# Performance work log

Hardware: AMD Instinct MI355X
Metric: run time of the kernel (lower is better)

## Reference

```python
import jax, jax.numpy as jnp
import numpy as np

N_NODES = 100000
N_EDGES = 1600000
F_IN = 128
HEADS1, CH1 = 8, 16
N_CLASSES = 64
NEG_SLOPE = 0.2  # PyG GATConv default leaky-relu slope


def setup_inputs() -> dict:
    key = jax.random.key(0)
    ks = jax.random.split(key, 10)
    x = jax.random.normal(ks[0], (N_NODES, F_IN), dtype=jnp.float32)
    edge_index = jax.random.randint(ks[1], (2, N_EDGES), 0, N_NODES, dtype=jnp.int32)
    s1 = 1.0 / np.sqrt(F_IN)
    s2 = 1.0 / np.sqrt(HEADS1 * CH1)
    W1 = jax.random.normal(ks[2], (F_IN, HEADS1 * CH1), dtype=jnp.float32) * s1
    a_src1 = jax.random.normal(ks[3], (HEADS1, CH1), dtype=jnp.float32) * s2
    a_dst1 = jax.random.normal(ks[4], (HEADS1, CH1), dtype=jnp.float32) * s2
    b1 = jnp.zeros((HEADS1 * CH1,), dtype=jnp.float32)
    W2 = jax.random.normal(ks[5], (HEADS1 * CH1, N_CLASSES), dtype=jnp.float32) * s2
    a_src2 = jax.random.normal(ks[6], (1, N_CLASSES), dtype=jnp.float32) * 0.1
    a_dst2 = jax.random.normal(ks[7], (1, N_CLASSES), dtype=jnp.float32) * 0.1
    b2 = jnp.zeros((N_CLASSES,), dtype=jnp.float32)
    return {"x": x, "edge_index": edge_index, "W1": W1, "a_src1": a_src1,
            "a_dst1": a_dst1, "b1": b1, "W2": W2, "a_src2": a_src2,
            "a_dst2": a_dst2, "b2": b2}


def gat_layer(x, src, dst, W, a_src, a_dst, b, heads, ch, concat):
    # PyG GATConv (eval mode, self-loops already appended to src/dst).
    N = x.shape[0]
    h = (x @ W).reshape(N, heads, ch)                      # [N,H,C]
    asn = jnp.einsum('nhc,hc->nh', h, a_src)               # src attention term
    adn = jnp.einsum('nhc,hc->nh', h, a_dst)               # dst attention term
    e = jax.nn.leaky_relu(asn[src] + adn[dst], NEG_SLOPE)  # [E,H]
    emax = jax.ops.segment_max(e, dst, num_segments=N)     # per-dst max (self-loops guarantee nonempty)
    ee = jnp.exp(e - emax[dst])
    denom = jax.ops.segment_sum(ee, dst, num_segments=N)
    alpha = ee / denom[dst]                                # segment softmax over incoming edges
    msg = h[src] * alpha[:, :, None]                       # [E,H,C]
    out = jax.ops.segment_sum(msg, dst, num_segments=N)    # [N,H,C]
    out = out.reshape(N, heads * ch) if concat else out.mean(axis=1)
    return out + b


def reference(x, edge_index, W1, a_src1, a_dst1, b1, W2, a_src2, a_dst2, b2):
    N = x.shape[0]
    loop = jnp.arange(N, dtype=edge_index.dtype)
    src = jnp.concatenate([edge_index[0], loop])  # add self-loops (PyG default)
    dst = jnp.concatenate([edge_index[1], loop])
    h = gat_layer(x, src, dst, W1, a_src1, a_dst1, b1, HEADS1, CH1, True)
    h = jax.nn.elu(h)
    # F.dropout with training=False is identity (eval mode)
    out = gat_layer(h, src, dst, W2, a_src2, a_dst2, b2, 1, N_CLASSES, False)
    return jax.nn.log_softmax(out, axis=1)
```

## Files before the change

### kernel.cpp

```cpp
#include <hip/hip_runtime.h>

#define NN 100000
#define NE 1600000
#define EN (NE + NN)
#define FIN 128
#define H1 8
#define C1 16
#define F1 128
#define NC 64
#define NEG 0.2f

#define BSH 7
#define BKN 128
#define NBUK ((NN + BKN - 1) / BKN)
#define NBLK 256
#define CHUNK ((EN + NBLK - 1) / NBLK)
__device__ __forceinline__ int chunk_of_block(int b) {
  return (b & 7) * (NBLK / 8) + (b >> 3);
}

typedef unsigned short ushort_t;
typedef unsigned int uint_t;
typedef __attribute__((ext_vector_type(8))) short short8v;
typedef __attribute__((ext_vector_type(4))) float f32x4;
typedef __attribute__((ext_vector_type(2))) float f32x2;

union U8 { ushort_t u[8]; short8v v; uint4 q; };

__device__ __forceinline__ ushort_t f2bf(float f) {
  uint_t u = __builtin_bit_cast(uint_t, f);
  u += 0x7FFF + ((u >> 16) & 1);
  return (ushort_t)(u >> 16);
}
__device__ __forceinline__ float bflo(uint_t u) {
  return __builtin_bit_cast(float, u << 16);
}
__device__ __forceinline__ float bfhi(uint_t u) {
  return __builtin_bit_cast(float, u & 0xFFFF0000u);
}

#if __has_builtin(__builtin_amdgcn_cvt_pk_fp8_f32) && \
    __has_builtin(__builtin_amdgcn_cvt_pk_f32_fp8)
__device__ __forceinline__ uint_t fp8_pack4(float f0, float f1, float f2,
                                            float f3) {
  int p = 0;
  p = __builtin_amdgcn_cvt_pk_fp8_f32(f0, f1, p, false);
  p = __builtin_amdgcn_cvt_pk_fp8_f32(f2, f3, p, true);
  return (uint_t)p;
}
__device__ __forceinline__ void fp8_unpack4(uint_t w, float* o) {
  f32x2 d0 = __builtin_amdgcn_cvt_pk_f32_fp8((int)w, false);
  f32x2 d1 = __builtin_amdgcn_cvt_pk_f32_fp8((int)w, true);
  o[0] = d0.x; o[1] = d0.y; o[2] = d1.x; o[3] = d1.y;
}
#else
__device__ __forceinline__ uint_t fp8_enc1(float f) {
  uint_t u = __builtin_bit_cast(uint_t, f);
  uint_t s = (u >> 24) & 0x80u;
  int e = (int)((u >> 23) & 0xFF) - 127;
  if (e < -9) return s;
  if (e < -6) {
    float af = __builtin_bit_cast(float, u & 0x7FFFFFFFu);
    uint_t m = (uint_t)(af * 512.f + 0.5f);
    return s | m;
  }
  uint_t mant = u & 0x7FFFFF;
  uint_t keep = mant >> 20;
  uint_t rest = mant & 0xFFFFF;
  keep += (rest > 0x80000u) || (rest == 0x80000u && (keep & 1));
  uint_t ee = (uint_t)(e + 7);
  if (keep == 8) { keep = 0; ee += 1; }
  if (ee > 15 || (ee == 15 && keep > 6)) return s | 0x7E;
  return s | (ee << 3) | keep;
}
__device__ __forceinline__ float fp8_dec1(uint_t b) {
  uint_t s = (b & 0x80u) << 24;
  uint_t e = (b >> 3) & 15u, m = b & 7u;
  if (e == 0) {
    float v = (float)m * (1.0f / 512.0f);
    return __builtin_bit_cast(float, s | __builtin_bit_cast(uint_t, v));
  }
  return __builtin_bit_cast(float, s | ((e + 120u) << 23) | (m << 20));
}
__device__ __forceinline__ uint_t fp8_pack4(float f0, float f1, float f2,
                                            float f3) {
  return fp8_enc1(f0) | (fp8_enc1(f1) << 8) | (fp8_enc1(f2) << 16) |
         (fp8_enc1(f3) << 24);
}
__device__ __forceinline__ void fp8_unpack4(uint_t w, float* o) {
  o[0] = fp8_dec1(w & 0xFF); o[1] = fp8_dec1((w >> 8) & 0xFF);
  o[2] = fp8_dec1((w >> 16) & 0xFF); o[3] = fp8_dec1(w >> 24);
}
#endif

__global__ __launch_bounds__(512) void bucket_count_kernel(
    const int* __restrict__ dstA, int* __restrict__ cnt,
    const float* __restrict__ W1, const float* __restrict__ W2,
    ushort_t* __restrict__ WT1, ushort_t* __restrict__ WT2) {
  __shared__ int histL[NBUK];
  int b = blockIdx.x, t = threadIdx.x;
  int gid = b * 512 + t;
  if (gid < 128 * 128) {
    int n = gid >> 7, k = gid & 127;
    int c = (n & 15) * 8 + (n >> 4);
    WT1[gid] = f2bf(W1[k * 128 + c]);
  } else if (gid < 128 * 128 + 64 * 128) {
    int j = gid - 128 * 128;
    int n = j >> 7, k = j & 127;
    int c = (n & 15) * 4 + (n >> 4);
    WT2[j] = f2bf(W2[k * 64 + c]);
  }
  for (int i = t; i < NBUK; i += 512) histL[i] = 0;
  __syncthreads();
  int ch = chunk_of_block(b);
  int e0 = ch * CHUNK, e1 = min(e0 + CHUNK, EN);
  for (int e = e0 + t; e < e1; e += 512) {
    int d = (e < NE) ? dstA[e] : (e - NE);
    atomicAdd(&histL[d >> BSH], 1);
  }
  __syncthreads();
  for (int i = t; i < NBUK; i += 512) cnt[i * NBLK + ch] = histL[i];
}

__global__ __launch_bounds__(256) void scan_chunks_kernel(
    int* __restrict__ cnt, int* __restrict__ colsum) {
  __shared__ int sd[2][256];
  int j = blockIdx.x, t = threadIdx.x;
  int v = cnt[j * NBLK + t];
  sd[0][t] = v;
  __syncthreads();
  int sp = 0;
  for (int off = 1; off < 256; off <<= 1) {
    int val = sd[sp][t];
    if (t >= off) val += sd[sp][t - off];
    sd[sp ^ 1][t] = val;
    __syncthreads();
    sp ^= 1;
  }
  cnt[j * NBLK + t] = sd[sp][t] - v;
  if (t == 255) colsum[j] = sd[sp][255];
}

__global__ __launch_bounds__(1024) void scan_buckets_kernel(
    const int* __restrict__ colsum, int* __restrict__ bucket_base) {
  __shared__ int sd[2][1024];
  int t = threadIdx.x;
  int v = (t < NBUK) ? colsum[t] : 0;
  sd[0][t] = v;
  __syncthreads();
  int sp = 0;
  for (int off = 1; off < 1024; off <<= 1) {
    int val = sd[sp][t];
    if (t >= off) val += sd[sp][t - off];
    sd[sp ^ 1][t] = val;
    __syncthreads();
    sp ^= 1;
  }
  if (t < NBUK) bucket_base[t] = sd[sp][t] - v;
  if (t == 0) bucket_base[NBUK] = EN;
}

__global__ __launch_bounds__(512) void scatter_gemm1_kernel(
    const int* __restrict__ srcA, const int* __restrict__ dstA,
    const int* __restrict__ cnt, const int* __restrict__ bucket_base,
    int* __restrict__ staging,
    const float* __restrict__ X, const ushort_t* __restrict__ WT1,
    const float* __restrict__ a_src, const float* __restrict__ a_dst,
    uint2* __restrict__ h8, float* __restrict__ asn, float* __restrict__ adn,
    int nrows) {
  __shared__ int cur[NBUK];
  if (blockIdx.x < NBLK) {
    int b = blockIdx.x, t = threadIdx.x;
    int ch = chunk_of_block(b);
    for (int i = t; i < NBUK; i += 512)
      cur[i] = cnt[i * NBLK + ch] + bucket_base[i];
    __syncthreads();
    int e0 = ch * CHUNK, e1 = min(e0 + CHUNK, EN);
    for (int e = e0 + t; e < e1; e += 512) {
      int s, d;
      if (e < NE) { s = srcA[e]; d = dstA[e]; } else { s = e - NE; d = s; }
      int pos = atomicAdd(&cur[d >> BSH], 1);
      staging[pos] = s | ((d & (BKN - 1)) << 17);
    }
    return;
  }
  const int tid = threadIdx.x;
  const int wave = tid >> 6, lane = tid & 63;
  const int row0 = (blockIdx.x - NBLK) * 128 + wave * 16;
  const int rlo = lane & 15, khi = lane >> 4;

  f32x4 acc[8];
#pragma unroll
  for (int n = 0; n < 8; ++n) acc[n] = (f32x4){0.f, 0.f, 0.f, 0.f};

#pragma unroll
  for (int ks = 0; ks < 4; ++ks) {
    const int kk = ks * 32 + khi * 8;
    int row = row0 + rlo;
    if (row >= nrows) row = nrows - 1;
    const float4* xp = (const float4*)(X + (size_t)row * 128 + kk);
    float4 u = xp[0], v = xp[1];
    U8 t;
    t.u[0] = f2bf(u.x); t.u[1] = f2bf(u.y); t.u[2] = f2bf(u.z); t.u[3] = f2bf(u.w);
    t.u[4] = f2bf(v.x); t.u[5] = f2bf(v.y); t.u[6] = f2bf(v.z); t.u[7] = f2bf(v.w);
    short8v a = t.v;
#pragma unroll
    for (int nf = 0; nf < 8; ++nf) {
      short8v b = *(const short8v*)(WT1 + (nf * 16 + rlo) * 128 + kk);
      acc[nf] = __builtin_amdgcn_mfma_f32_16x16x32_bf16(a, b, acc[nf], 0, 0, 0);
    }
  }
  const float4* as4 = (const float4*)a_src;
  const float4* ad4 = (const float4*)a_dst;
  float4 as0 = as4[rlo * 2], as1 = as4[rlo * 2 + 1];
  float4 ad0 = ad4[rlo * 2], ad1 = ad4[rlo * 2 + 1];
  int rbase = row0 + khi * 4;
#pragma unroll
  for (int r = 0; r < 4; ++r) {
    int row = rbase + r;
    bool ok = (row < nrows);
    uint2 pk;
    pk.x = fp8_pack4(acc[0][r], acc[1][r], acc[2][r], acc[3][r]);
    pk.y = fp8_pack4(acc[4][r], acc[5][r], acc[6][r], acc[7][r]);
    if (ok) h8[(size_t)row * 16 + rlo] = pk;
    float s = acc[0][r] * as0.x + acc[1][r] * as0.y +
              acc[2][r] * as0.z + acc[3][r] * as0.w +
              acc[4][r] * as1.x + acc[5][r] * as1.y +
              acc[6][r] * as1.z + acc[7][r] * as1.w;
    float d = acc[0][r] * ad0.x + acc[1][r] * ad0.y +
              acc[2][r] * ad0.z + acc[3][r] * ad0.w +
              acc[4][r] * ad1.x + acc[5][r] * ad1.y +
              acc[6][r] * ad1.z + acc[7][r] * ad1.w;
    s += __shfl_xor(s, 1);
    d += __shfl_xor(d, 1);
    if (ok && (rlo & 1) == 0) {
      asn[row * 8 + (rlo >> 1)] = s;
      adn[row * 8 + (rlo >> 1)] = d;
    }
  }
}

__global__ __launch_bounds__(1024) void csr_gather1_kernel(
    const int* __restrict__ staging, const int* __restrict__ bucket_base,
    int* __restrict__ rp, int* __restrict__ col,
    const float* __restrict__ asn, const float* __restrict__ adn,
    const uint4* __restrict__ h8, const float* __restrict__ b1,
    ushort_t* __restrict__ x2) {
  __shared__ int degL[BKN];
  __shared__ int curL[BKN];
  __shared__ int startL[BKN + 1];
  __shared__ int sdata[2][BKN];
  int bk = blockIdx.x, t = threadIdx.x;
  int ebase = bucket_base[bk], eend = bucket_base[bk + 1];
  int ecnt = eend - ebase;
  if (t < BKN) degL[t] = 0;
  __syncthreads();
  for (int e = t; e < ecnt; e += 1024)
    atomicAdd(&degL[staging[ebase + e] >> 17], 1);
  __syncthreads();
  if (t < BKN) sdata[0][t] = degL[t];
  __syncthreads();
  int sp = 0;
  for (int off = 1; off < BKN; off <<= 1) {
    if (t < BKN) {
      int val = sdata[sp][t];
      if (t >= off) val += sdata[sp][t - off];
      sdata[sp ^ 1][t] = val;
    }
    __syncthreads();
    sp ^= 1;
  }
  if (t < BKN) {
    int ex = sdata[sp][t] - degL[t];
    curL[t] = ex;
    startL[t] = ebase + ex;
    int node = bk * BKN + t;
    if (node < NN) rp[node] = ebase + ex;
  }
  if (t == 0) startL[BKN] = eend;
  if (bk == 0 && t == 0) rp[NN] = EN;
  __syncthreads();
  for (int e = t; e < ecnt; e += 1024) {
    int pk = staging[ebase + e];
    int pos = atomicAdd(&curL[pk >> 17], 1);
    col[ebase + pos] = pk & 0x1FFFF;
  }
  __syncthreads();
  int i = t >> 3, lane = t & 7;
  int node = bk * BKN + i;
  if (node >= NN) return;
  float aD = adn[node * 8 + lane];
  int p = startL[i], p1 = startL[i + 1];
  float a[16];
#pragma unroll
  for (int j = 0; j < 16; ++j) a[j] = 0.f;
  float den = 0.f;
  for (; p + 1 < p1; p += 2) {
    int s0 = col[p], s1 = col[p + 1];
    float e0 = asn[s0 * 8 + lane] + aD;
    float e1 = asn[s1 * 8 + lane] + aD;
    uint4 q0 = h8[(size_t)s0 * 8 + lane];
    uint4 q1 = h8[(size_t)s1 * 8 + lane];
    e0 = e0 > 0.f ? e0 : NEG * e0;
    e1 = e1 > 0.f ? e1 : NEG * e1;
    float ee0 = __expf(e0), ee1 = __expf(e1);
    float d0[4], d1[4], d2[4], d3[4];
    fp8_unpack4(q0.x, d0); fp8_unpack4(q0.y, d1);
    fp8_unpack4(q0.z, d2); fp8_unpack4(q0.w, d3);
    float g0[4], g1[4], g2[4], g3[4];
    fp8_unpack4(q1.x, g0); fp8_unpack4(q1.y, g1);
    fp8_unpack4(q1.z, g2); fp8_unpack4(q1.w, g3);
#pragma unroll
    for (int j = 0; j < 4; ++j) {
      a[j]      += ee0 * d0[j] + ee1 * g0[j];
      a[4 + j]  += ee0 * d1[j] + ee1 * g1[j];
      a[8 + j]  += ee0 * d2[j] + ee1 * g2[j];
      a[12 + j] += ee0 * d3[j] + ee1 * g3[j];
    }
    den += ee0 + ee1;
  }
  if (p < p1) {
    int s0 = col[p];
    float e0 = asn[s0 * 8 + lane] + aD;
    uint4 q0 = h8[(size_t)s0 * 8 + lane];
    e0 = e0 > 0.f ? e0 : NEG * e0;
    float ee0 = __expf(e0);
    float d0[4], d1[4], d2[4], d3[4];
    fp8_unpack4(q0.x, d0); fp8_unpack4(q0.y, d1);
    fp8_unpack4(q0.z, d2); fp8_unpack4(q0.w, d3);
#pragma unroll
    for (int j = 0; j < 4; ++j) {
      a[j] += ee0 * d0[j];
      a[4 + j] += ee0 * d1[j];
      a[8 + j] += ee0 * d2[j];
      a[12 + j] += ee0 * d3[j];
    }
    den += ee0;
  }
  float inv = 1.f / den;
  const float4* b4 = (const float4*)b1;
  U8 t0, t1;
#pragma unroll
  for (int h = 0; h < 4; ++h) {
    float4 bv = b4[lane * 4 + h];
    float o0 = fmaf(a[h * 4 + 0], inv, bv.x);
    float o1 = fmaf(a[h * 4 + 1], inv, bv.y);
    float o2 = fmaf(a[h * 4 + 2], inv, bv.z);
    float o3 = fmaf(a[h * 4 + 3], inv, bv.w);
    o0 = o0 > 0.f ? o0 : __expf(o0) - 1.f;
    o1 = o1 > 0.f ? o1 : __expf(o1) - 1.f;
    o2 = o2 > 0.f ? o2 : __expf(o2) - 1.f;
    o3 = o3 > 0.f ? o3 : __expf(o3) - 1.f;
    U8& tt = (h < 2) ? t0 : t1;
    int base = (h & 1) * 4;
    tt.u[base + 0] = f2bf(o0); tt.u[base + 1] = f2bf(o1);
    tt.u[base + 2] = f2bf(o2); tt.u[base + 3] = f2bf(o3);
  }
  uint4* xr = (uint4*)(x2 + (size_t)node * F1);
  xr[lane * 2 + 0] = t0.q;
  xr[lane * 2 + 1] = t1.q;
}

__global__ __launch_bounds__(256) void mfma_gemm2_kernel(
    const ushort_t* __restrict__ X2, const ushort_t* __restrict__ WT2,
    const float* __restrict__ a_src, const float* __restrict__ a_dst,
    uint_t* __restrict__ h28, float* __restrict__ asn, float* __restrict__ adn,
    int nrows) {
  const int tid = threadIdx.x;
  const int wave = tid >> 6, lane = tid & 63;
  const int row0 = blockIdx.x * 64 + wave * 16;
  const int rlo = lane & 15, khi = lane >> 4;

  f32x4 acc[4];
#pragma unroll
  for (int n = 0; n < 4; ++n) acc[n] = (f32x4){0.f, 0.f, 0.f, 0.f};

#pragma unroll
  for (int ks = 0; ks < 4; ++ks) {
    const int kk = ks * 32 + khi * 8;
    int row = row0 + rlo;
    if (row >= nrows) row = nrows - 1;
    U8 t;
    t.q = *(const uint4*)(X2 + (size_t)row * 128 + kk);
    short8v a = t.v;
#pragma unroll
    for (int nf = 0; nf < 4; ++nf) {
      short8v b = *(const short8v*)(WT2 + (nf * 16 + rlo) * 128 + kk);
      acc[nf] = __builtin_amdgcn_mfma_f32_16x16x32_bf16(a, b, acc[nf], 0, 0, 0);
    }
  }
  float4 as = ((const float4*)a_src)[rlo];
  float4 ad = ((const float4*)a_dst)[rlo];
  int rbase = row0 + khi * 4;
#pragma unroll
  for (int r = 0; r < 4; ++r) {
    int row = rbase + r;
    bool ok = (row < nrows);
    uint_t pk = fp8_pack4(acc[0][r], acc[1][r], acc[2][r], acc[3][r]);
    if (ok) h28[(size_t)row * 16 + rlo] = pk;
    float s = acc[0][r] * as.x + acc[1][r] * as.y +
              acc[2][r] * as.z + acc[3][r] * as.w;
    float d = acc[0][r] * ad.x + acc[1][r] * ad.y +
              acc[2][r] * ad.z + acc[3][r] * ad.w;
    s += __shfl_xor(s, 1); s += __shfl_xor(s, 2);
    s += __shfl_xor(s, 4); s += __shfl_xor(s, 8);
    d += __shfl_xor(d, 1); d += __shfl_xor(d, 2);
    d += __shfl_xor(d, 4); d += __shfl_xor(d, 8);
    if (ok && rlo == 0) { asn[row] = s; adn[row] = d; }
  }
}

__global__ __launch_bounds__(256) void gather2_kernel(
    const int* __restrict__ rp, const int* __restrict__ col,
    const float* __restrict__ asn, const float* __restrict__ adn,
    const uint2* __restrict__ h28, const float* __restrict__ b2,
    float* __restrict__ out) {
  int node = (blockIdx.x << 5) + (threadIdx.x >> 3);
  if (node >= NN) return;
  int lane = threadIdx.x & 7;
  float aD = adn[node];
  int p = rp[node], p1 = rp[node + 1];
  float a[8];
#pragma unroll
  for (int j = 0; j < 8; ++j) a[j] = 0.f;
  float den = 0.f;

  for (; p + 1 < p1; p += 2) {
    int s0 = col[p], s1 = col[p + 1];
    float e0 = asn[s0] + aD;
    float e1 = asn[s1] + aD;
    uint2 q0 = h28[(size_t)s0 * 8 + lane];
    uint2 q1 = h28[(size_t)s1 * 8 + lane];
    e0 = e0 > 0.f ? e0 : NEG * e0;
    e1 = e1 > 0.f ? e1 : NEG * e1;
    float ee0 = __expf(e0), ee1 = __expf(e1);
    float d0[4], d1[4], g0[4], g1[4];
    fp8_unpack4(q0.x, d0); fp8_unpack4(q0.y, d1);
    fp8_unpack4(q1.x, g0); fp8_unpack4(q1.y, g1);
#pragma unroll
    for (int j = 0; j < 4; ++j) {
      a[j] += ee0 * d0[j] + ee1 * g0[j];
      a[4 + j] += ee0 * d1[j] + ee1 * g1[j];
    }
    den += ee0 + ee1;
  }
  if (p < p1) {
    int s0 = col[p];
    float e0 = asn[s0] + aD;
    uint2 q0 = h28[(size_t)s0 * 8 + lane];
    e0 = e0 > 0.f ? e0 : NEG * e0;
    float ee0 = __expf(e0);
    float d0[4], d1[4];
    fp8_unpack4(q0.x, d0); fp8_unpack4(q0.y, d1);
#pragma unroll
    for (int j = 0; j < 4; ++j) {
      a[j] += ee0 * d0[j];
      a[4 + j] += ee0 * d1[j];
    }
    den += ee0;
  }
  float inv = 1.f / den;
  float4 bv0 = ((const float4*)b2)[lane * 2 + 0];
  float4 bv1 = ((const float4*)b2)[lane * 2 + 1];
  float v[8];
  v[0] = fmaf(a[0], inv, bv0.x); v[1] = fmaf(a[1], inv, bv0.y);
  v[2] = fmaf(a[2], inv, bv0.z); v[3] = fmaf(a[3], inv, bv0.w);
  v[4] = fmaf(a[4], inv, bv1.x); v[5] = fmaf(a[5], inv, bv1.y);
  v[6] = fmaf(a[6], inv, bv1.z); v[7] = fmaf(a[7], inv, bv1.w);
  float m = v[0];
#pragma unroll
  for (int j = 1; j < 8; ++j) m = fmaxf(m, v[j]);
#pragma unroll
  for (int k = 1; k < 8; k <<= 1) m = fmaxf(m, __shfl_xor(m, k));
  float ex = 0.f;
#pragma unroll
  for (int j = 0; j < 8; ++j) ex += __expf(v[j] - m);
#pragma unroll
  for (int k = 1; k < 8; k <<= 1) ex += __shfl_xor(ex, k);
  float lse = m + __logf(ex);
  float4 r0 = {v[0] - lse, v[1] - lse, v[2] - lse, v[3] - lse};
  float4 r1 = {v[4] - lse, v[5] - lse, v[6] - lse, v[7] - lse};
  float4* orow = (float4*)(out + (size_t)node * NC);
  orow[lane * 2 + 0] = r0;
  orow[lane * 2 + 1] = r1;
}

extern "C" void kernel_launch(void* const* d_in, const int* in_sizes, int n_in,
                              void* d_out, int out_size, void* d_ws,
                              size_t ws_size, hipStream_t stream) {
  const float* x = (const float*)d_in[0];
  const int* edge_index = (const int*)d_in[1];
  const float* W1 = (const float*)d_in[2];
  const float* a_src1 = (const float*)d_in[3];
  const float* a_dst1 = (const float*)d_in[4];
  const float* b1 = (const float*)d_in[5];
  const float* W2 = (const float*)d_in[6];
  const float* a_src2 = (const float*)d_in[7];
  const float* a_dst2 = (const float*)d_in[8];
  const float* b2 = (const float*)d_in[9];
  float* out = (float*)d_out;
  float* ws = (float*)d_ws;

  ushort_t* x2b = (ushort_t*)ws;
  uint4* h8 = (uint4*)(ws + 6400000);
  uint2* h28 = (uint2*)(ws + 9600000);
  float* asn1 = ws + 11200000;
  float* adn1 = ws + 12000000;
  float* asn2 = ws + 12800000;
  float* adn2 = ws + 12900000;
  ushort_t* WT1 = (ushort_t*)(ws + 13000000);
  ushort_t* WT2 = (ushort_t*)(ws + 13010000);
  int* rp = (int*)(ws + 13020000);
  int* col = rp + NN + 1;
  int* staging = col + EN;
  int* cnt = staging + EN;
  int* bucket_base = cnt + NBUK * NBLK;
  int* colsum = bucket_base + NBUK + 1;

  const int* srcA = edge_index;
  const int* dstA = edge_index + NE;

  bucket_count_kernel<<<NBLK, 512, 0, stream>>>(dstA, cnt, W1, W2, WT1, WT2);
  scan_chunks_kernel<<<NBUK, 256, 0, stream>>>(cnt, colsum);
  scan_buckets_kernel<<<1, 1024, 0, stream>>>(colsum, bucket_base);
  scatter_gemm1_kernel<<<NBLK + (NN + 127) / 128, 512, 0, stream>>>(
      srcA, dstA, cnt, bucket_base, staging, x, WT1, a_src1, a_dst1,
      (uint2*)h8, asn1, adn1, NN);
  csr_gather1_kernel<<<NBUK, 1024, 0, stream>>>(staging, bucket_base, rp, col,
                                                asn1, adn1, h8, b1, x2b);
  mfma_gemm2_kernel<<<(NN + 63) / 64, 256, 0, stream>>>(
      x2b, WT2, a_src2, a_dst2, (uint_t*)h28, asn2, adn2, NN);
  gather2_kernel<<<(NN + 31) / 32, 256, 0, stream>>>(rp, col, asn2, adn2, h28,
                                                     b2, out);
}
```

Before: 189.0 us.

## Split scatter from GEMM1 and stage bucket CSR columns in LDS

Splits the fused scatter+GEMM1 kernel into two separate launches: a scatter kernel and a 256-thread GEMM1 kernel over 64-row tiles. In the CSR/gather kernel, each bucket's column list is built in shared memory when it fits (CAPB entries). The gather loop then reads source indices from LDS rather than re-reading global col. This is meant to remove the global round-trip of col and the scattered writes. In exchange it adds an extra kernel launch, loses the overlap between scatter and GEMM, and larger LDS use may lower occupancy of the 1024-thread blocks.

```diff
diff --git a/kernel.cpp b/kernel.cpp
--- a/kernel.cpp
+++ b/kernel.cpp
@@ -15,6 +15,7 @@
 #define NBUK ((NN + BKN - 1) / BKN)
 #define NBLK 256
 #define CHUNK ((EN + NBLK - 1) / NBLK)
+#define CAPB 2688
 __device__ __forceinline__ int chunk_of_block(int b) {
   return (b & 7) * (NBLK / 8) + (b >> 3);
 }
@@ -160,33 +161,33 @@
   if (t == 0) bucket_base[NBUK] = EN;
 }
 
-__global__ __launch_bounds__(512) void scatter_gemm1_kernel(
+__global__ __launch_bounds__(512) void bucket_scatter_kernel(
     const int* __restrict__ srcA, const int* __restrict__ dstA,
     const int* __restrict__ cnt, const int* __restrict__ bucket_base,
-    int* __restrict__ staging,
+    int* __restrict__ staging) {
+  __shared__ int cur[NBUK];
+  int b = blockIdx.x, t = threadIdx.x;
+  int ch = chunk_of_block(b);
+  for (int i = t; i < NBUK; i += 512)
+    cur[i] = cnt[i * NBLK + ch] + bucket_base[i];
+  __syncthreads();
+  int e0 = ch * CHUNK, e1 = min(e0 + CHUNK, EN);
+  for (int e = e0 + t; e < e1; e += 512) {
+    int s, d;
+    if (e < NE) { s = srcA[e]; d = dstA[e]; } else { s = e - NE; d = s; }
+    int pos = atomicAdd(&cur[d >> BSH], 1);
+    staging[pos] = s | ((d & (BKN - 1)) << 17);
+  }
+}
+
+__global__ __launch_bounds__(256) void mfma_gemm1_kernel(
     const float* __restrict__ X, const ushort_t* __restrict__ WT1,
     const float* __restrict__ a_src, const float* __restrict__ a_dst,
     uint2* __restrict__ h8, float* __restrict__ asn, float* __restrict__ adn,
     int nrows) {
-  __shared__ int cur[NBUK];
-  if (blockIdx.x < NBLK) {
-    int b = blockIdx.x, t = threadIdx.x;
-    int ch = chunk_of_block(b);
-    for (int i = t; i < NBUK; i += 512)
-      cur[i] = cnt[i * NBLK + ch] + bucket_base[i];
-    __syncthreads();
-    int e0 = ch * CHUNK, e1 = min(e0 + CHUNK, EN);
-    for (int e = e0 + t; e < e1; e += 512) {
-      int s, d;
-      if (e < NE) { s = srcA[e]; d = dstA[e]; } else { s = e - NE; d = s; }
-      int pos = atomicAdd(&cur[d >> BSH], 1);
-      staging[pos] = s | ((d & (BKN - 1)) << 17);
-    }
-    return;
-  }
   const int tid = threadIdx.x;
   const int wave = tid >> 6, lane = tid & 63;
-  const int row0 = (blockIdx.x - NBLK) * 128 + wave * 16;
+  const int row0 = blockIdx.x * 64 + wave * 16;
   const int rlo = lane & 15, khi = lane >> 4;
 
   f32x4 acc[8];
@@ -250,9 +251,11 @@
   __shared__ int curL[BKN];
   __shared__ int startL[BKN + 1];
   __shared__ int sdata[2][BKN];
+  __shared__ int colL[CAPB];
   int bk = blockIdx.x, t = threadIdx.x;
   int ebase = bucket_base[bk], eend = bucket_base[bk + 1];
   int ecnt = eend - ebase;
+  bool fits = (ecnt <= CAPB);
   if (t < BKN) degL[t] = 0;
   __syncthreads();
   for (int e = t; e < ecnt; e += 1024)
@@ -273,17 +276,28 @@
   if (t < BKN) {
     int ex = sdata[sp][t] - degL[t];
     curL[t] = ex;
-    startL[t] = ebase + ex;
+    startL[t] = ex;
     int node = bk * BKN + t;
     if (node < NN) rp[node] = ebase + ex;
   }
-  if (t == 0) startL[BKN] = eend;
+  if (t == 0) startL[BKN] = ecnt;
   if (bk == 0 && t == 0) rp[NN] = EN;
   __syncthreads();
-  for (int e = t; e < ecnt; e += 1024) {
-    int pk = staging[ebase + e];
-    int pos = atomicAdd(&curL[pk >> 17], 1);
-    col[ebase + pos] = pk & 0x1FFFF;
+  if (fits) {
+    for (int e = t; e < ecnt; e += 1024) {
+      int pk = staging[ebase + e];
+      int pos = atomicAdd(&curL[pk >> 17], 1);
+      colL[pos] = pk & 0x1FFFF;
+    }
+    __syncthreads();
+    for (int e = t; e < ecnt; e += 1024) col[ebase + e] = colL[e];
+  } else {
+    for (int e = t; e < ecnt; e += 1024) {
+      int pk = staging[ebase + e];
+      int pos = atomicAdd(&curL[pk >> 17], 1);
+      col[ebase + pos] = pk & 0x1FFFF;
+    }
+    __syncthreads();
   }
   __syncthreads();
   int i = t >> 3, lane = t & 7;
@@ -295,47 +309,69 @@
 #pragma unroll
   for (int j = 0; j < 16; ++j) a[j] = 0.f;
   float den = 0.f;
-  for (; p + 1 < p1; p += 2) {
-    int s0 = col[p], s1 = col[p + 1];
-    float e0 = asn[s0 * 8 + lane] + aD;
-    float e1 = asn[s1 * 8 + lane] + aD;
-    uint4 q0 = h8[(size_t)s0 * 8 + lane];
-    uint4 q1 = h8[(size_t)s1 * 8 + lane];
-    e0 = e0 > 0.f ? e0 : NEG * e0;
-    e1 = e1 > 0.f ? e1 : NEG * e1;
-    float ee0 = __expf(e0), ee1 = __expf(e1);
-    float d0[4], d1[4], d2[4], d3[4];
-    fp8_unpack4(q0.x, d0); fp8_unpack4(q0.y, d1);
-    fp8_unpack4(q0.z, d2); fp8_unpack4(q0.w, d3);
-    float g0[4], g1[4], g2[4], g3[4];
-    fp8_unpack4(q1.x, g0); fp8_unpack4(q1.y, g1);
-    fp8_unpack4(q1.z, g2); fp8_unpack4(q1.w, g3);
-#pragma unroll
-    for (int j = 0; j < 4; ++j) {
-      a[j]      += ee0 * d0[j] + ee1 * g0[j];
-      a[4 + j]  += ee0 * d1[j] + ee1 * g1[j];
-      a[8 + j]  += ee0 * d2[j] + ee1 * g2[j];
-      a[12 + j] += ee0 * d3[j] + ee1 * g3[j];
-    }
-    den += ee0 + ee1;
-  }
-  if (p < p1) {
-    int s0 = col[p];
-    float e0 = asn[s0 * 8 + lane] + aD;
-    uint4 q0 = h8[(size_t)s0 * 8 + lane];
-    e0 = e0 > 0.f ? e0 : NEG * e0;
-    float ee0 = __expf(e0);
-    float d0[4], d1[4], d2[4], d3[4];
-    fp8_unpack4(q0.x, d0); fp8_unpack4(q0.y, d1);
-    fp8_unpack4(q0.z, d2); fp8_unpack4(q0.w, d3);
-#pragma unroll
-    for (int j = 0; j < 4; ++j) {
-      a[j] += ee0 * d0[j];
-      a[4 + j] += ee0 * d1[j];
-      a[8 + j] += ee0 * d2[j];
-      a[12 + j] += ee0 * d3[j];
-    }
-    den += ee0;
+  if (fits) {
+    for (; p + 1 < p1; p += 2) {
+      int s0 = colL[p], s1 = colL[p + 1];
+      float e0 = asn[s0 * 8 + lane] + aD;
+      float e1 = asn[s1 * 8 + lane] + aD;
+      uint4 q0 = h8[(size_t)s0 * 8 + lane];
+      uint4 q1 = h8[(size_t)s1 * 8 + lane];
+      e0 = e0 > 0.f ? e0 : NEG * e0;
+      e1 = e1 > 0.f ? e1 : NEG * e1;
+      float ee0 = __expf(e0), ee1 = __expf(e1);
+      float d0[4], d1[4], d2[4], d3[4];
+      fp8_unpack4(q0.x, d0); fp8_unpack4(q0.y, d1);
+      fp8_unpack4(q0.z, d2); fp8_unpack4(q0.w, d3);
+      float g0[4], g1[4], g2[4], g3[4];
+      fp8_unpack4(q1.x, g0); fp8_unpack4(q1.y, g1);
+      fp8_unpack4(q1.z, g2); fp8_unpack4(q1.w, g3);
+#pragma unroll
+      for (int j = 0; j < 4; ++j) {
+        a[j]      += ee0 * d0[j] + ee1 * g0[j];
+        a[4 + j]  += ee0 * d1[j] + ee1 * g1[j];
+        a[8 + j]  += ee0 * d2[j] + ee1 * g2[j];
+        a[12 + j] += ee0 * d3[j] + ee1 * g3[j];
+      }
+      den += ee0 + ee1;
+    }
+    if (p < p1) {
+      int s0 = colL[p];
+      float e0 = asn[s0 * 8 + lane] + aD;
+      uint4 q0 = h8[(size_t)s0 * 8 + lane];
+      e0 = e0 > 0.f ? e0 : NEG * e0;
+      float ee0 = __expf(e0);
+      float d0[4], d1[4], d2[4], d3[4];
+      fp8_unpack4(q0.x, d0); fp8_unpack4(q0.y, d1);
+      fp8_unpack4(q0.z, d2); fp8_unpack4(q0.w, d3);
+#pragma unroll
+      for (int j = 0; j < 4; ++j) {
+        a[j] += ee0 * d0[j];
+        a[4 + j] += ee0 * d1[j];
+        a[8 + j] += ee0 * d2[j];
+        a[12 + j] += ee0 * d3[j];
+      }
+      den += ee0;
+    }
+  } else {
+    const int* cg = col + ebase;
+    for (; p < p1; ++p) {
+      int s0 = cg[p];
+      float e0 = asn[s0 * 8 + lane] + aD;
+      uint4 q0 = h8[(size_t)s0 * 8 + lane];
+      e0 = e0 > 0.f ? e0 : NEG * e0;
+      float ee0 = __expf(e0);
+      float d0[4], d1[4], d2[4], d3[4];
+      fp8_unpack4(q0.x, d0); fp8_unpack4(q0.y, d1);
+      fp8_unpack4(q0.z, d2); fp8_unpack4(q0.w, d3);
+#pragma unroll
+      for (int j = 0; j < 4; ++j) {
+        a[j] += ee0 * d0[j];
+        a[4 + j] += ee0 * d1[j];
+        a[8 + j] += ee0 * d2[j];
+        a[12 + j] += ee0 * d3[j];
+      }
+      den += ee0;
+    }
   }
   float inv = 1.f / den;
   const float4* b4 = (const float4*)b1;
@@ -523,9 +559,10 @@
   bucket_count_kernel<<<NBLK, 512, 0, stream>>>(dstA, cnt, W1, W2, WT1, WT2);
   scan_chunks_kernel<<<NBUK, 256, 0, stream>>>(cnt, colsum);
   scan_buckets_kernel<<<1, 1024, 0, stream>>>(colsum, bucket_base);
-  scatter_gemm1_kernel<<<NBLK + (NN + 127) / 128, 512, 0, stream>>>(
-      srcA, dstA, cnt, bucket_base, staging, x, WT1, a_src1, a_dst1,
-      (uint2*)h8, asn1, adn1, NN);
+  bucket_scatter_kernel<<<NBLK, 512, 0, stream>>>(srcA, dstA, cnt, bucket_base,
+                                                  staging);
+  mfma_gemm1_kernel<<<(NN + 63) / 64, 256, 0, stream>>>(
+      x, WT1, a_src1, a_dst1, (uint2*)h8, asn1, adn1, NN);
   csr_gather1_kernel<<<NBUK, 1024, 0, stream>>>(staging, bucket_base, rp, col,
                                                 asn1, adn1, h8, b1, x2b);
   mfma_gemm2_kernel<<<(NN + 63) / 64, 256, 0, stream>>>(
```

Result: faster. 176.9 us (-6.4%).
